# Kernel tuning notes

Measured on AMD Instinct MI355X. Metric: run time of the kernel, lower is better.

Reference implementation:

```python
import jax, jax.numpy as jnp
import numpy as np
from jax import lax

H = W = 512
NT = 1000


def setup_inputs() -> dict:
    key = jax.random.key(0)
    kx, ky = jax.random.split(key)
    X = jax.random.uniform(kx, (H, W), dtype=jnp.float32)
    Y = jax.random.uniform(ky, (H, W), dtype=jnp.float32)
    return {"X": X, "Y": Y}


def reference(X, Y):
    # Gaussian initial condition, same math as torch.exp(-50*((X-0.5)^2+(Y-0.5)^2))
    x0 = jnp.exp(-50.0 * ((X - 0.5) ** 2 + (Y - 0.5) ** 2))
    h, w = x0.shape
    # mask zeroing the boundary (rows/cols 0 and -1)
    mask = jnp.zeros((h, w), dtype=x0.dtype).at[1:-1, 1:-1].set(1.0)

    def step(x, _):
        # 3x3 cross kernel [[0,.25,0],[.25,0,.25],[0,.25,0]] with zero padding=1,
        # expressed as four shifted adds (identical math, no conv launch overhead)
        p = jnp.pad(x, 1)
        xn = 0.25 * (p[:-2, 1:-1] + p[2:, 1:-1] + p[1:-1, :-2] + p[1:-1, 2:])
        return xn * mask, None

    x, _ = lax.scan(step, x0, None, length=NT)
    # original returns NCHW with N=C=1
    return x[None, None]
```

## Files before the change

### kernel.cpp

```cpp
#include <hip/hip_runtime.h>
#include <math.h>


#define HW 512
#define NP 128

__device__ __forceinline__ int mode_of(int p) {
    return (p < 64) ? (p + 1) : (p + 383);
}

__device__ __forceinline__ float gauss(const float* __restrict__ X,
                                       const float* __restrict__ Y, int idx) {
    float dx = X[idx] - 0.5f, dy = Y[idx] - 0.5f;
    return expf(-50.0f * (dx * dx + dy * dy));
}

__global__ void k_prep(const float* __restrict__ X, const float* __restrict__ Y,
                       float* __restrict__ x1, float* __restrict__ S,
                       float* __restrict__ ST, float* __restrict__ L,
                       float* __restrict__ C1) {
    int b = blockIdx.x, t = threadIdx.x;
    if (b < 1024) {
        int idx = b * 256 + t;
        int i = idx >> 9, j = idx & 511;
        float v = 0.0f;
        if (i > 0 && i < HW - 1 && j > 0 && j < HW - 1) {
            v = 0.25f * (gauss(X, Y, idx - HW) + gauss(X, Y, idx + HW) +
                         gauss(X, Y, idx - 1)  + gauss(X, Y, idx + 1));
        }
        x1[idx] = v;
    } else if (b < 1280) {
        int idx = (b - 1024) * 256 + t;
        int p = idx >> 9, i = idx & 511;
        long tt = ((long)mode_of(p) * (long)i) % 1022;
        S[idx] = (float)sin((double)tt * (M_PI / 511.0));
    } else if (b < 1536) {
        int idx = (b - 1280) * 256 + t;
        int i = idx >> 7, p = idx & 127;
        long tt = ((long)mode_of(p) * (long)i) % 1022;
        ST[idx] = (float)sin((double)tt * (M_PI / 511.0));
    } else if (b < 1600) {
        int idx = (b - 1536) * 256 + t;
        int p = idx >> 7, q = idx & 127;
        double lp = cos((double)mode_of(p) * M_PI / 511.0);
        double lq = cos((double)mode_of(q) * M_PI / 511.0);
        double lam = 0.5 * (lp + lq);
        double mag = pow(fabs(lam), 999.0);
        if (lam < 0.0) mag = -mag;
        L[idx] = (float)(mag * (2.0 / 511.0) * (2.0 / 511.0));
    } else {
        ((float4*)C1)[(b - 1600) * 256 + t] = float4{0.f, 0.f, 0.f, 0.f};
    }
}

__global__ void k_m1(const float* __restrict__ S, const float* __restrict__ x1,
                     float* __restrict__ C1) {
    int j = blockIdx.x * 256 + threadIdx.x;
    int p0 = blockIdx.y * 4;
    int i0 = blockIdx.z * 64;
    const float* S0 = S + p0 * HW + i0;
    const float* S1 = S0 + HW;
    const float* S2 = S1 + HW;
    const float* S3 = S2 + HW;
    const float* xp = x1 + i0 * HW + j;
    float a0 = 0.f, a1 = 0.f, a2 = 0.f, a3 = 0.f;
    #pragma unroll 8
    for (int i = 0; i < 64; i++) {
        float x = xp[i * HW];
        a0 += S0[i] * x;
        a1 += S1[i] * x;
        a2 += S2[i] * x;
        a3 += S3[i] * x;
    }
    unsafeAtomicAdd(&C1[(p0 + 0) * HW + j], a0);
    unsafeAtomicAdd(&C1[(p0 + 1) * HW + j], a1);
    unsafeAtomicAdd(&C1[(p0 + 2) * HW + j], a2);
    unsafeAtomicAdd(&C1[(p0 + 3) * HW + j], a3);
}

__global__ void k_m23(const float* __restrict__ C1, const float* __restrict__ ST,
                      const float* __restrict__ L, const float* __restrict__ S,
                      float* __restrict__ E) {
    __shared__ float c1[HW];
    __shared__ float drow[NP];
    int p = blockIdx.x, t = threadIdx.x;
    #pragma unroll
    for (int k = 0; k < 4; k++) c1[t + k * NP] = C1[p * HW + t + k * NP];
    __syncthreads();
    float b0 = 0.f, b1 = 0.f, b2 = 0.f, b3 = 0.f;
    #pragma unroll 8
    for (int j = 0; j < HW; j += 4) {
        b0 += c1[j + 0] * ST[(j + 0) * NP + t];
        b1 += c1[j + 1] * ST[(j + 1) * NP + t];
        b2 += c1[j + 2] * ST[(j + 2) * NP + t];
        b3 += c1[j + 3] * ST[(j + 3) * NP + t];
    }
    drow[t] = ((b0 + b1) + (b2 + b3)) * L[p * NP + t];
    __syncthreads();
    float e0 = 0.f, e1 = 0.f, e2 = 0.f, e3 = 0.f;
    #pragma unroll 8
    for (int q = 0; q < NP; q++) {
        float d = drow[q];
        const float* Sq = S + q * HW + t;
        e0 += d * Sq[0];
        e1 += d * Sq[128];
        e2 += d * Sq[256];
        e3 += d * Sq[384];
    }
    E[p * HW + t + 0]   = e0;
    E[p * HW + t + 128] = e1;
    E[p * HW + t + 256] = e2;
    E[p * HW + t + 384] = e3;
}

__global__ void k_m4(const float* __restrict__ S, const float* __restrict__ E,
                     float* __restrict__ out) {
    int j = blockIdx.x * 256 + threadIdx.x;
    int i0 = blockIdx.y * 4;
    float a0 = 0.f, a1 = 0.f, a2 = 0.f, a3 = 0.f;
    #pragma unroll 16
    for (int p = 0; p < NP; p++) {
        float e = E[p * HW + j];
        a0 += S[p * HW + i0 + 0] * e;
        a1 += S[p * HW + i0 + 1] * e;
        a2 += S[p * HW + i0 + 2] * e;
        a3 += S[p * HW + i0 + 3] * e;
    }
    out[(i0 + 0) * HW + j] = a0;
    out[(i0 + 1) * HW + j] = a1;
    out[(i0 + 2) * HW + j] = a2;
    out[(i0 + 3) * HW + j] = a3;
}


extern "C" void kernel_launch(void* const* d_in, const int* in_sizes, int n_in,
                              void* d_out, int out_size, void* d_ws, size_t ws_size,
                              hipStream_t stream) {
    const float* X = (const float*)d_in[0];
    const float* Y = (const float*)d_in[1];
    float* out = (float*)d_out;

    float* ws = (float*)d_ws;
    float* x1 = ws;
    float* S  = x1 + HW * HW;
    float* ST = S + NP * HW;
    float* L  = ST + HW * NP;
    float* C1 = L + NP * NP;
    float* E  = C1 + NP * HW;

    k_prep<<<dim3(1664),        dim3(256), 0, stream>>>(X, Y, x1, S, ST, L, C1);
    k_m1  <<<dim3(2, 32, 8),    dim3(256), 0, stream>>>(S, x1, C1);
    k_m23 <<<dim3(NP),          dim3(128), 0, stream>>>(C1, ST, L, S, E);
    k_m4  <<<dim3(2, 128),      dim3(256), 0, stream>>>(S, E, out);
}
```

Before: 85.85 us.

## Replace atomics with partial buffers, exploit sine symmetry, widen stencil-projection kernels

The first projection kernel now writes per-slice partial sums to a workspace buffer instead of using atomic adds. This removes the need to zero C1 in the prep kernel. The second kernel reduces those partials and uses 512 threads with a shared-memory split reduction, which gives more parallelism per block. The prep kernel computes half the sine table and fills the mirrored modes by symmetry. It also replaces pow with square-and-multiply and drops the C1-zeroing blocks. The trade-off is extra workspace traffic for the partial buffer and more synchronisation steps inside k_m23.

```diff
diff --git a/kernel.cpp b/kernel.cpp
--- a/kernel.cpp
+++ b/kernel.cpp
@@ -17,8 +17,7 @@
 
 __global__ void k_prep(const float* __restrict__ X, const float* __restrict__ Y,
                        float* __restrict__ x1, float* __restrict__ S,
-                       float* __restrict__ ST, float* __restrict__ L,
-                       float* __restrict__ C1) {
+                       float* __restrict__ ST, float* __restrict__ L) {
     int b = blockIdx.x, t = threadIdx.x;
     if (b < 1024) {
         int idx = b * 256 + t;
@@ -29,88 +28,98 @@
                          gauss(X, Y, idx - 1)  + gauss(X, Y, idx + 1));
         }
         x1[idx] = v;
+    } else if (b < 1152) {
+        int idx = (b - 1024) * 256 + t;
+        int pa = idx >> 9, i = idx & 511;
+        long tt = ((long)(pa + 1) * (long)i) % 1022;
+        float s = (float)sin((double)tt * (M_PI / 511.0));
+        S[pa * HW + i] = s;
+        S[(127 - pa) * HW + i] = (i & 1) ? s : -s;
     } else if (b < 1280) {
-        int idx = (b - 1024) * 256 + t;
-        int p = idx >> 9, i = idx & 511;
-        long tt = ((long)mode_of(p) * (long)i) % 1022;
-        S[idx] = (float)sin((double)tt * (M_PI / 511.0));
-    } else if (b < 1536) {
+        int idx = (b - 1152) * 256 + t;
+        int i = idx >> 6, pa = idx & 63;
+        long tt = ((long)(pa + 1) * (long)i) % 1022;
+        float s = (float)sin((double)tt * (M_PI / 511.0));
+        ST[i * NP + pa] = s;
+        ST[i * NP + (127 - pa)] = (i & 1) ? s : -s;
+    } else {
         int idx = (b - 1280) * 256 + t;
-        int i = idx >> 7, p = idx & 127;
-        long tt = ((long)mode_of(p) * (long)i) % 1022;
-        ST[idx] = (float)sin((double)tt * (M_PI / 511.0));
-    } else if (b < 1600) {
-        int idx = (b - 1536) * 256 + t;
         int p = idx >> 7, q = idx & 127;
         double lp = cos((double)mode_of(p) * M_PI / 511.0);
         double lq = cos((double)mode_of(q) * M_PI / 511.0);
         double lam = 0.5 * (lp + lq);
-        double mag = pow(fabs(lam), 999.0);
-        if (lam < 0.0) mag = -mag;
-        L[idx] = (float)(mag * (2.0 / 511.0) * (2.0 / 511.0));
-    } else {
-        ((float4*)C1)[(b - 1600) * 256 + t] = float4{0.f, 0.f, 0.f, 0.f};
+        double r = 1.0, base = fabs(lam);
+        int e = 999;
+        #pragma unroll
+        for (int k = 0; k < 10; k++) {
+            if (e & 1) r *= base;
+            base *= base;
+            e >>= 1;
+        }
+        if (lam < 0.0) r = -r;
+        L[idx] = (float)(r * (2.0 / 511.0) * (2.0 / 511.0));
     }
 }
 
 __global__ void k_m1(const float* __restrict__ S, const float* __restrict__ x1,
-                     float* __restrict__ C1) {
+                     float* __restrict__ P) {
     int j = blockIdx.x * 256 + threadIdx.x;
-    int p0 = blockIdx.y * 4;
-    int i0 = blockIdx.z * 64;
-    const float* S0 = S + p0 * HW + i0;
-    const float* S1 = S0 + HW;
-    const float* S2 = S1 + HW;
-    const float* S3 = S2 + HW;
+    int p0 = blockIdx.y * 8;
+    int iz = blockIdx.z;
+    int i0 = iz * 64;
+    const float* Sb = S + p0 * HW + i0;
     const float* xp = x1 + i0 * HW + j;
-    float a0 = 0.f, a1 = 0.f, a2 = 0.f, a3 = 0.f;
+    float a[8] = {0.f, 0.f, 0.f, 0.f, 0.f, 0.f, 0.f, 0.f};
     #pragma unroll 8
     for (int i = 0; i < 64; i++) {
         float x = xp[i * HW];
-        a0 += S0[i] * x;
-        a1 += S1[i] * x;
-        a2 += S2[i] * x;
-        a3 += S3[i] * x;
+        #pragma unroll
+        for (int k = 0; k < 8; k++) a[k] += Sb[k * HW + i] * x;
     }
-    unsafeAtomicAdd(&C1[(p0 + 0) * HW + j], a0);
-    unsafeAtomicAdd(&C1[(p0 + 1) * HW + j], a1);
-    unsafeAtomicAdd(&C1[(p0 + 2) * HW + j], a2);
-    unsafeAtomicAdd(&C1[(p0 + 3) * HW + j], a3);
+    float* Pp = P + iz * NP * HW + p0 * HW + j;
+    #pragma unroll
+    for (int k = 0; k < 8; k++) Pp[k * HW] = a[k];
 }
 
-__global__ void k_m23(const float* __restrict__ C1, const float* __restrict__ ST,
+__global__ void k_m23(const float* __restrict__ P, const float* __restrict__ ST,
                       const float* __restrict__ L, const float* __restrict__ S,
                       float* __restrict__ E) {
     __shared__ float c1[HW];
+    __shared__ float part[512];
     __shared__ float drow[NP];
     int p = blockIdx.x, t = threadIdx.x;
-    #pragma unroll
-    for (int k = 0; k < 4; k++) c1[t + k * NP] = C1[p * HW + t + k * NP];
+    {
+        const float* Pp = P + p * HW + t;
+        float s0 = 0.f, s1 = 0.f;
+        #pragma unroll
+        for (int iz = 0; iz < 8; iz += 2) {
+            s0 += Pp[iz * NP * HW];
+            s1 += Pp[(iz + 1) * NP * HW];
+        }
+        c1[t] = s0 + s1;
+    }
     __syncthreads();
-    float b0 = 0.f, b1 = 0.f, b2 = 0.f, b3 = 0.f;
+    int q = t & 127, jg = t >> 7;
+    const float* STp = ST + (jg * 128) * NP + q;
+    const float* cc = c1 + jg * 128;
+    float b0 = 0.f, b1 = 0.f;
     #pragma unroll 8
-    for (int j = 0; j < HW; j += 4) {
-        b0 += c1[j + 0] * ST[(j + 0) * NP + t];
-        b1 += c1[j + 1] * ST[(j + 1) * NP + t];
-        b2 += c1[j + 2] * ST[(j + 2) * NP + t];
-        b3 += c1[j + 3] * ST[(j + 3) * NP + t];
+    for (int j = 0; j < 128; j += 2) {
+        b0 += cc[j] * STp[j * NP];
+        b1 += cc[j + 1] * STp[(j + 1) * NP];
     }
-    drow[t] = ((b0 + b1) + (b2 + b3)) * L[p * NP + t];
+    part[t] = b0 + b1;
     __syncthreads();
-    float e0 = 0.f, e1 = 0.f, e2 = 0.f, e3 = 0.f;
+    if (t < NP)
+        drow[t] = (part[t] + part[t + 128] + part[t + 256] + part[t + 384]) * L[p * NP + t];
+    __syncthreads();
+    float e0 = 0.f, e1 = 0.f;
     #pragma unroll 8
-    for (int q = 0; q < NP; q++) {
-        float d = drow[q];
-        const float* Sq = S + q * HW + t;
-        e0 += d * Sq[0];
-        e1 += d * Sq[128];
-        e2 += d * Sq[256];
-        e3 += d * Sq[384];
+    for (int qq = 0; qq < NP; qq += 2) {
+        e0 += drow[qq] * S[qq * HW + t];
+        e1 += drow[qq + 1] * S[(qq + 1) * HW + t];
     }
-    E[p * HW + t + 0]   = e0;
-    E[p * HW + t + 128] = e1;
-    E[p * HW + t + 256] = e2;
-    E[p * HW + t + 384] = e3;
+    E[p * HW + t] = e0 + e1;
 }
 
 __global__ void k_m4(const float* __restrict__ S, const float* __restrict__ E,
@@ -145,11 +154,11 @@
     float* S  = x1 + HW * HW;
     float* ST = S + NP * HW;
     float* L  = ST + HW * NP;
-    float* C1 = L + NP * NP;
-    float* E  = C1 + NP * HW;
+    float* E  = L + NP * NP;
+    float* P  = E + NP * HW;
 
-    k_prep<<<dim3(1664),        dim3(256), 0, stream>>>(X, Y, x1, S, ST, L, C1);
-    k_m1  <<<dim3(2, 32, 8),    dim3(256), 0, stream>>>(S, x1, C1);
-    k_m23 <<<dim3(NP),          dim3(128), 0, stream>>>(C1, ST, L, S, E);
+    k_prep<<<dim3(1344),        dim3(256), 0, stream>>>(X, Y, x1, S, ST, L);
+    k_m1  <<<dim3(2, 16, 8),    dim3(256), 0, stream>>>(S, x1, P);
+    k_m23 <<<dim3(NP),          dim3(512), 0, stream>>>(P, ST, L, S, E);
     k_m4  <<<dim3(2, 128),      dim3(256), 0, stream>>>(S, E, out);
 }
```

Measured after the change: 80.63 us. 1.06x faster.
